# Kernel tuning notes

Hardware: AMD Instinct MI355X
Metric: run time of the kernel (lower is better)

Reference implementation:

```python
import jax, jax.numpy as jnp
import numpy as np

NUM_EMBEDDINGS = 8192
EMA_DECAY = 0.99


def setup_inputs() -> dict:
    key = jax.random.key(0)
    k1, k2 = jax.random.split(key)
    encodings = jax.random.normal(k1, (16, 128, 32, 32), dtype=jnp.float32)
    weight = 0.02 * jax.random.normal(k2, (NUM_EMBEDDINGS, 128), dtype=jnp.float32)
    return {"encodings": encodings, "weight": weight}


def reference(encodings, weight):
    B, C, H, W = encodings.shape
    K = weight.shape[0]
    # [B, C, H, W] -> [N, C], N = B*H*W
    x = encodings.transpose(0, 2, 3, 1).reshape(-1, C)
    # pairwise squared distances via norms + matmul: [N, K]
    dist = (
        jnp.sum(x * x, axis=1, keepdims=True)
        + jnp.sum(weight * weight, axis=1)[None, :]
        - 2.0 * jnp.matmul(x, weight.T)
    )
    quantized_ids = jnp.argmin(dist, axis=1)  # [N] int
    # straight-through estimator
    q = x + jax.lax.stop_gradient(weight[quantized_ids] - x)  # [N, C]
    # training-mode EMA codebook update (scatter-add counts and sums)
    counts = jax.ops.segment_sum(
        jnp.ones((x.shape[0],), dtype=x.dtype), quantized_ids, num_segments=K
    )
    sums = jax.ops.segment_sum(x, quantized_ids, num_segments=K)
    new_means = sums / (counts[:, None] + 1e-12)
    new_weight = EMA_DECAY * weight + (1.0 - EMA_DECAY) * new_means
    ids_out = quantized_ids.reshape(B, H, W)
    q_out = q.reshape(B, H, W, C).transpose(0, 3, 1, 2)  # [B, C, H, W]
    return ids_out, q_out, new_weight
```

## Files before the change

### kernel.cpp

```cpp
#include <hip/hip_runtime.h>
#include <stdint.h>
#include <stddef.h>


#define N_ROWS   16384
#define K_CODES  8192
#define C_DIM    128

typedef _Float16 f16x8 __attribute__((ext_vector_type(8)));
typedef float    f32x4 __attribute__((ext_vector_type(4)));

__global__ __launch_bounds__(256) void prep(const float* __restrict__ enc,
                                            const float* __restrict__ w,
                                            _Float16* __restrict__ Ap,
                                            _Float16* __restrict__ Bp,
                                            float* __restrict__ xT,
                                            float* __restrict__ xnorm,
                                            float* __restrict__ wnorm,
                                            float* __restrict__ wnmax128) {
  __shared__ float t[128][65];
  const int tid = threadIdx.x;
  if (blockIdx.x < 256) {
    const int b = blockIdx.x >> 4;
    const int hw0 = (blockIdx.x & 15) << 6;
    #pragma unroll
    for (int i = 0; i < 32; ++i) {
      int idx = i * 256 + tid;
      int c = idx >> 6, hwl = idx & 63;
      t[c][hwl] = enc[((size_t)(b * 128 + c) << 10) + hw0 + hwl];
    }
    __syncthreads();
    const int r = tid >> 2, sub = tid & 3;
    const int n = (b << 10) + hw0 + r;
    const int R = n >> 4, m = n & 15;
    float s = 0.f;
    #pragma unroll
    for (int q = 0; q < 4; ++q) {
      f16x8 hv;
      float vv[8];
      #pragma unroll
      for (int e = 0; e < 8; ++e) {
        float v = t[sub * 32 + q * 8 + e][r];
        vv[e] = v;
        s += v * v;
        hv[e] = (_Float16)v;
      }
      *(f16x8*)(Ap + ((size_t)(R * 4 + sub) * 64 + (m + 16 * q)) * 8) = hv;
      *(float4*)(xT + (size_t)n * 128 + sub * 32 + q * 8) =
          (float4){vv[0], vv[1], vv[2], vv[3]};
      *(float4*)(xT + (size_t)n * 128 + sub * 32 + q * 8 + 4) =
          (float4){vv[4], vv[5], vv[6], vv[7]};
    }
    s += __shfl_xor(s, 1);
    s += __shfl_xor(s, 2);
    if (sub == 0) xnorm[n] = s;
  } else {
    __shared__ float wred[4];
    const int kk = (blockIdx.x - 256) * 64 + (tid >> 2), sub = tid & 3;
    const int R = kk >> 4, m = kk & 15;
    const float* base = w + (size_t)kk * C_DIM + sub * 32;
    float s = 0.f;
    #pragma unroll
    for (int q = 0; q < 4; ++q) {
      f16x8 hv;
      float4 va = *(const float4*)(base + q * 8);
      float4 vb = *(const float4*)(base + q * 8 + 4);
      float vv[8] = {va.x, va.y, va.z, va.w, vb.x, vb.y, vb.z, vb.w};
      #pragma unroll
      for (int e = 0; e < 8; ++e) { s += vv[e] * vv[e]; hv[e] = (_Float16)vv[e]; }
      *(f16x8*)(Bp + ((size_t)(R * 4 + sub) * 64 + (m + 16 * q)) * 8) = hv;
    }
    s += __shfl_xor(s, 1);
    s += __shfl_xor(s, 2);
    if (sub == 0) wnorm[kk] = s;
    float wx = s;
    #pragma unroll
    for (int st = 1; st <= 32; st <<= 1) wx = fmaxf(wx, __shfl_xor(wx, st));
    if ((tid & 63) == 0) wred[tid >> 6] = wx;
    __syncthreads();
    if (tid == 0)
      wnmax128[blockIdx.x - 256] =
          fmaxf(fmaxf(wred[0], wred[1]), fmaxf(wred[2], wred[3]));
  }
}

__global__ __launch_bounds__(512) void gemm_argmin(
    const _Float16* __restrict__ Ap, const _Float16* __restrict__ Bp,
    const float* __restrict__ wnorm,
    float* __restrict__ pd1, float* __restrict__ pd2,
    unsigned* __restrict__ icount, unsigned* __restrict__ fcount)
{
  __shared__ _Float16 sbuf[2][8192];
  const int tid = threadIdx.x;
  const int lane = tid & 63, wave = tid >> 6;
  const int m = lane & 15, q = lane >> 4;
  const int cs = blockIdx.x;
  const int row0 = blockIdx.y * 128;
  const int Tr = blockIdx.y * 8 + wave;

  if (cs == 0 && blockIdx.y == 0 && tid == 0) {
    *icount = 0u; *fcount = 0u;
  }

#define STAGE(b, hgn) do {                                                   \
    const size_t bh_ = ((size_t)((cs * 64 + (hgn) * 4) * 4) << 9);           \
    _Pragma("unroll")                                                        \
    for (int r_ = 0; r_ < 2; ++r_) {                                         \
      __builtin_amdgcn_global_load_lds(                                      \
          (const __attribute__((address_space(1))) void*)                    \
              (Bp + bh_ + ((size_t)(r_ * 512 + tid) << 3)),                  \
          (__attribute__((address_space(3))) void*)                          \
              (&sbuf[b][(r_ * 512 + tid) << 3]),                             \
          16, 0, 0);                                                         \
    }                                                                        \
  } while (0)

  f16x8 bx[4];
  #pragma unroll
  for (int kc = 0; kc < 4; ++kc)
    bx[kc] = *(const f16x8*)(Ap + (((size_t)Tr * 4 + kc) << 9) + (lane << 3));
  const int row = row0 + wave * 16 + m;
  const unsigned q5 = (unsigned)(q << 5);

  STAGE(0, 0);

  float c1 = 0.f, c2 = 0.f;
  for (int hg = 0; hg < 16; ++hg) {
    __syncthreads();
    if (hg < 15) STAGE((hg + 1) & 1, hg + 1);
    const _Float16* fb = &sbuf[hg & 1][0];
    const int half = hg & 1;
    f32x4 acc[4];
    #pragma unroll
    for (int t = 0; t < 4; ++t) acc[t] = (f32x4){0.f, 0.f, 0.f, 0.f};
    #pragma unroll
    for (int kc = 0; kc < 4; ++kc) {
      #pragma unroll
      for (int t = 0; t < 4; ++t) {
        f16x8 a = *(const f16x8*)(fb + ((t * 4 + kc) << 9) + (lane << 3));
        acc[t] = __builtin_amdgcn_mfma_f32_16x16x32_f16(a, bx[kc], acc[t], 0, 0, 0);
      }
    }
    float m1t[4], m2t[4];
    #pragma unroll
    for (int t = 0; t < 4; ++t) {
      const int tj = half * 4 + t;
      const int cb = (cs * 64 + hg * 4 + t) * 16 + 4 * q;
      float4 wnq = *(const float4*)(wnorm + cb);
      unsigned b0 = __float_as_uint(fmaf(-2.0f, acc[t][0], wnq.x)) & 0xFFFFFF80u;
      unsigned b1 = __float_as_uint(fmaf(-2.0f, acc[t][1], wnq.y)) & 0xFFFFFF80u;
      unsigned b2 = __float_as_uint(fmaf(-2.0f, acc[t][2], wnq.z)) & 0xFFFFFF80u;
      unsigned b3 = __float_as_uint(fmaf(-2.0f, acc[t][3], wnq.w)) & 0xFFFFFF80u;
      float v0 = __uint_as_float(b0);
      float v1 = __uint_as_float(b1 | 1u);
      float v2 = __uint_as_float(b2 | 2u);
      float v3 = __uint_as_float(b3 | 3u);
      float l1 = fminf(v0, v1), h1 = fmaxf(v0, v1);
      float l2 = fminf(v2, v3), h2 = fmaxf(v2, v3);
      float mm1 = fminf(l1, l2);
      float mm2 = fminf(fminf(h1, h2), fmaxf(l1, l2));
      m1t[t] = __uint_as_float(__float_as_uint(mm1) | (unsigned)(tj << 2));
      m2t[t] = mm2;
    }
    m2t[0] = fminf(fminf(m2t[0], m2t[1]), fmaxf(m1t[0], m1t[1]));
    m1t[0] = fminf(m1t[0], m1t[1]);
    m2t[2] = fminf(fminf(m2t[2], m2t[3]), fmaxf(m1t[2], m1t[3]));
    m1t[2] = fminf(m1t[2], m1t[3]);
    m2t[0] = fminf(fminf(m2t[0], m2t[2]), fmaxf(m1t[0], m1t[2]));
    m1t[0] = fminf(m1t[0], m1t[2]);
    if (half == 0) {
      c1 = m1t[0]; c2 = m2t[0];
    } else {
      c2 = fminf(fminf(c2, m2t[0]), fmaxf(c1, m1t[0]));
      c1 = fminf(c1, m1t[0]);
      float d1 = __uint_as_float(__float_as_uint(c1) | q5);
      float d2 = c2;
      #pragma unroll
      for (int s = 16; s <= 32; s <<= 1) {
        float o1 = __shfl_xor(d1, s), o2 = __shfl_xor(d2, s);
        d2 = fminf(fminf(d2, o2), fmaxf(d1, o1));
        d1 = fminf(d1, o1);
      }
      if (q == 0) {
        const int g = cs * 8 + (hg >> 1);
        size_t pi = (size_t)g * N_ROWS + row;
        pd1[pi] = d1;
        pd2[pi] = d2;
      }
    }
  }
#undef STAGE
}

__global__ __launch_bounds__(256) void classify(
    const float* __restrict__ pd1, const float* __restrict__ pd2,
    const float* __restrict__ xnorm, const float* __restrict__ wnmax128,
    int* __restrict__ ids, unsigned* __restrict__ items,
    unsigned* __restrict__ icount, int* __restrict__ fulll,
    unsigned* __restrict__ fcount, unsigned long long* __restrict__ keys,
    unsigned* __restrict__ cnt)
{
  __shared__ float wred[4];
  const int tid = threadIdx.x;
  const int gidx = blockIdx.x * 256 + tid;
  const int row = gidx >> 2, p = gidx & 3;
  if (p == 0) keys[row] = ~0ull;
  if (gidx < K_CODES) cnt[gidx] = 0u;
  float wv = wnmax128[tid & 127];
  #pragma unroll
  for (int st = 1; st <= 32; st <<= 1) wv = fmaxf(wv, __shfl_xor(wv, st));
  if ((tid & 63) == 0) wred[tid >> 6] = wv;
  __syncthreads();
  const float wm = fmaxf(fmaxf(wred[0], wred[1]), fmaxf(wred[2], wred[3]));

  float v1[16];
  float lmin = __builtin_inff();
  #pragma unroll
  for (int j = 0; j < 16; ++j) {
    v1[j] = pd1[(size_t)(p * 16 + j) * N_ROWS + row];
    lmin = fminf(lmin, v1[j]);
  }
  lmin = fminf(lmin, __shfl_xor(lmin, 1));
  lmin = fminf(lmin, __shfl_xor(lmin, 2));
  float twoE = 2.0f * (0.0029297f * sqrtf(xnorm[row] * wm) + 5e-4f);
  float T = lmin + twoE;
  bool full = false;
  int nc = 0;
  unsigned cands[6];
  #pragma unroll
  for (int j = 0; j < 16; ++j) {
    size_t i = (size_t)(p * 16 + j) * N_ROWS + row;
    if (pd2[i] <= T) { full = true; }
    else if (v1[j] <= T) {
      if (nc < 6) {
        unsigned ui = __float_as_uint(v1[j]) & 127u;
        unsigned g = (unsigned)(p * 16 + j);
        cands[nc++] = (g << 7) | (((ui >> 2) & 7u) << 4) |
                      ((ui >> 5) << 2) | (ui & 3u);
      } else full = true;
    }
  }
  unsigned fm = full ? 1u : 0u;
  int nct = nc;
  fm |= (unsigned)__shfl_xor((int)fm, 1); nct += __shfl_xor(nct, 1);
  fm |= (unsigned)__shfl_xor((int)fm, 2); nct += __shfl_xor(nct, 2);
  if (nct > 6) fm = 1u;
  if (fm) {
    if (p == 0) { unsigned fi = atomicAdd(fcount, 1u); fulll[fi] = row; }
  } else if (nct >= 2) {
    if (nc > 0) {
      unsigned base = atomicAdd(icount, (unsigned)nc);
      for (int i2 = 0; i2 < nc; ++i2)
        items[base + i2] = ((unsigned)row << 13) | cands[i2];
    }
  } else if (nc == 1) {
    ids[row] = (int)cands[0];
  }
}

__global__ __launch_bounds__(256) void refine(
    const float* __restrict__ xT, const float* __restrict__ w,
    const float* __restrict__ xnorm, const float* __restrict__ wnorm,
    const unsigned* __restrict__ items, const unsigned* __restrict__ icount,
    const int* __restrict__ fulll, const unsigned* __restrict__ fcount,
    unsigned long long* __restrict__ keys) {
  const int tid = threadIdx.x;
  const int lane = tid & 63, wave = tid >> 6;
  const unsigned ic = *icount;
  for (unsigned i = blockIdx.x * 256 + tid; i < ic; i += gridDim.x * 256) {
    unsigned it = items[i];
    int row = (int)(it >> 13), c = (int)(it & 8191u);
    const float* xb = xT + (size_t)row * C_DIM;
    const float* wk = w + (size_t)c * C_DIM;
    float s = 0.f;
    #pragma unroll 8
    for (int c4 = 0; c4 < 32; ++c4) {
      float4 xv = *(const float4*)(xb + c4 * 4);
      float4 wv = *(const float4*)(wk + c4 * 4);
      s = fmaf(xv.x, wv.x, s);
      s = fmaf(xv.y, wv.y, s);
      s = fmaf(xv.z, wv.z, s);
      s = fmaf(xv.w, wv.w, s);
    }
    float d = (xnorm[row] + wnorm[c]) - 2.0f * s;
    unsigned sb = __float_as_uint(d);
    sb = (sb >> 31) ? ~sb : (sb | 0x80000000u);
    unsigned long long key = ((unsigned long long)sb << 32) | (unsigned)c;
    atomicMin(&keys[row], key);
  }
  __shared__ __align__(16) float xs[128];
  __shared__ unsigned long long red[4];
  const unsigned nitems = *fcount * 8;
  for (unsigned item = blockIdx.x; item < nitems; item += gridDim.x) {
    const int row = fulll[item >> 3];
    const int slice = (int)(item & 7u);
    if (tid < 128)
      xs[tid] = xT[(size_t)row * C_DIM + tid];
    __syncthreads();
    const float xn = xnorm[row];
    const int k0 = slice * 1024 + tid * 4;
    float S[4];
    #pragma unroll
    for (int j = 0; j < 4; ++j) S[j] = 0.f;
    for (int c4 = 0; c4 < 32; ++c4) {
      float4 xv = *(const float4*)(&xs[c4 * 4]);
      #pragma unroll
      for (int j = 0; j < 4; ++j) {
        float4 wv = *(const float4*)(w + (size_t)(k0 + j) * C_DIM + c4 * 4);
        S[j] = fmaf(xv.x, wv.x, S[j]);
        S[j] = fmaf(xv.y, wv.y, S[j]);
        S[j] = fmaf(xv.z, wv.z, S[j]);
        S[j] = fmaf(xv.w, wv.w, S[j]);
      }
    }
    unsigned long long best = ~0ull;
    #pragma unroll
    for (int j = 0; j < 4; ++j) {
      float d = (xn + wnorm[k0 + j]) - 2.0f * S[j];
      unsigned sb = __float_as_uint(d);
      sb = (sb >> 31) ? ~sb : (sb | 0x80000000u);
      unsigned long long key = ((unsigned long long)sb << 32) | (unsigned)(k0 + j);
      best = best < key ? best : key;
    }
    #pragma unroll
    for (int s = 1; s <= 32; s <<= 1) {
      unsigned long long ok = __shfl_xor(best, s);
      best = ok < best ? ok : best;
    }
    if (lane == 0) red[wave] = best;
    __syncthreads();
    if (tid == 0) {
      unsigned long long bk = red[0];
      #pragma unroll
      for (int wv = 1; wv < 4; ++wv) bk = red[wv] < bk ? red[wv] : bk;
      atomicMin(&keys[row], bk);
    }
    __syncthreads();
  }
}

__global__ void resolve_ids(const unsigned long long* __restrict__ keys,
                            int* __restrict__ ids, unsigned* __restrict__ cnt,
                            float* __restrict__ out_ids) {
  int row = blockIdx.x * 256 + threadIdx.x;
  unsigned long long k = keys[row];
  int id = (k != ~0ull) ? (int)(unsigned)(k & 0xffffffffu) : ids[row];
  ids[row] = id;
  out_ids[row] = (float)id;
  atomicAdd(&cnt[id], 1u);
}

__global__ __launch_bounds__(256) void scan_offsets(
    const unsigned* __restrict__ cnt,
    unsigned* __restrict__ offs, unsigned* __restrict__ cursor) {
  __shared__ unsigned tot[256];
  const int tid = threadIdx.x;
  unsigned local[32], run = 0;
  #pragma unroll
  for (int i = 0; i < 32; ++i) { local[i] = run; run += cnt[tid * 32 + i]; }
  tot[tid] = run;
  __syncthreads();
  for (int st = 1; st < 256; st <<= 1) {
    unsigned v = (tid >= st) ? tot[tid - st] : 0u;
    __syncthreads();
    tot[tid] += v;
    __syncthreads();
  }
  unsigned excl = (tid == 0) ? 0u : tot[tid - 1];
  #pragma unroll
  for (int i = 0; i < 32; ++i) {
    unsigned o = excl + local[i];
    offs[tid * 32 + i] = o;
    cursor[tid * 32 + i] = o;
  }
}

__global__ void fill_rowlist(const int* __restrict__ ids,
                             unsigned* __restrict__ cursor,
                             int* __restrict__ rowlist) {
  int row = blockIdx.x * 256 + threadIdx.x;
  unsigned slot = atomicAdd(&cursor[ids[row]], 1u);
  rowlist[slot] = row;
}

__global__ __launch_bounds__(256) void qsum_final(
    const float* __restrict__ enc, const float* __restrict__ w,
    const int* __restrict__ ids,
    const unsigned* __restrict__ cnt, const unsigned* __restrict__ offs,
    const int* __restrict__ rowlist, const float* __restrict__ xT,
    float* __restrict__ outq, float* __restrict__ outw) {
  if (blockIdx.x < 2048) {
    int e = blockIdx.x * 1024 + threadIdx.x * 4;
    int c = (e >> 10) & 127;
    int b = e >> 17;
    int n = (b << 10) | (e & 1023);
    float4 x = *(const float4*)(enc + e);
    float4 o;
    o.x = x.x + (w[(size_t)ids[n + 0] * C_DIM + c] - x.x);
    o.y = x.y + (w[(size_t)ids[n + 1] * C_DIM + c] - x.y);
    o.z = x.z + (w[(size_t)ids[n + 2] * C_DIM + c] - x.z);
    o.w = x.w + (w[(size_t)ids[n + 3] * C_DIM + c] - x.w);
    *(float4*)(outq + e) = o;
  } else {
    const int tid = threadIdx.x;
    const int lane = tid & 63, wave = tid >> 6;
    const int k = (int)(blockIdx.x - 2048) * 4 + wave;
    const unsigned n0 = offs[k], nk = cnt[k];
    float S0a = 0.f, S0b = 0.f, S0c = 0.f, S0d = 0.f;
    float S1a = 0.f, S1b = 0.f, S1c = 0.f, S1d = 0.f;
    unsigned i = 0;
    for (; i + 4 <= nk; i += 4) {
      int r0 = rowlist[n0 + i],     r1 = rowlist[n0 + i + 1];
      int r2 = rowlist[n0 + i + 2], r3 = rowlist[n0 + i + 3];
      S0a += xT[(size_t)r0 * 128 + lane];      S1a += xT[(size_t)r0 * 128 + lane + 64];
      S0b += xT[(size_t)r1 * 128 + lane];      S1b += xT[(size_t)r1 * 128 + lane + 64];
      S0c += xT[(size_t)r2 * 128 + lane];      S1c += xT[(size_t)r2 * 128 + lane + 64];
      S0d += xT[(size_t)r3 * 128 + lane];      S1d += xT[(size_t)r3 * 128 + lane + 64];
    }
    for (; i < nk; ++i) {
      int r = rowlist[n0 + i];
      S0a += xT[(size_t)r * 128 + lane];
      S1a += xT[(size_t)r * 128 + lane + 64];
    }
    float S0 = (S0a + S0b) + (S0c + S0d);
    float S1 = (S1a + S1b) + (S1c + S1d);
    const float omd = (float)(1.0 - 0.99);
    float cf = (float)nk + 1e-12f;
    outw[(size_t)k * 128 + lane]      = 0.99f * w[(size_t)k * 128 + lane]      + omd * (S0 / cf);
    outw[(size_t)k * 128 + lane + 64] = 0.99f * w[(size_t)k * 128 + lane + 64] + omd * (S1 / cf);
  }
}

extern "C" void kernel_launch(void* const* d_in, const int* in_sizes, int n_in,
                              void* d_out, int out_size, void* d_ws, size_t ws_size,
                              hipStream_t stream) {
  const float* enc = (const float*)d_in[0];
  const float* w   = (const float*)d_in[1];
  float* out = (float*)d_out;
  float* out_ids = out;
  float* out_q   = out + N_ROWS;
  float* out_w   = out + N_ROWS + N_ROWS * C_DIM;

  char* ws = (char*)d_ws;
  _Float16* Ap  = (_Float16*)(ws);
  _Float16* Bp  = (_Float16*)(ws + 4194304);
  float* xnorm  = (float*)(ws + 6291456);
  float* wnorm  = (float*)(ws + 6356992);
  float* pd1    = (float*)(ws + 6389760);
  float* pd2    = (float*)(ws + 10584064);
  float* wnmax128 = (float*)(ws + 14778368);
  int* ids      = (int*)(ws + 18972672);
  int* fulll    = (int*)(ws + 19038208);
  unsigned* items = (unsigned*)(ws + 19103744);
  unsigned* icount = (unsigned*)(ws + 20152324);
  unsigned* fcount = (unsigned*)(ws + 20152328);
  unsigned* cnt    = (unsigned*)(ws + 20152336);
  unsigned* offs   = (unsigned*)(ws + 20185104);
  unsigned* cursor = (unsigned*)(ws + 20217872);
  unsigned long long* keys = (unsigned long long*)(ws + 20250640);
  int* rowlist  = (int*)(ws + 20381712);
  float* xT     = (float*)(ws + 20447248);
  (void)in_sizes; (void)n_in; (void)out_size; (void)ws_size;


  prep<<<384, 256, 0, stream>>>(enc, w, Ap, Bp, xT, xnorm, wnorm, wnmax128);
  gemm_argmin<<<dim3(8, N_ROWS / 128), 512, 0, stream>>>(
      Ap, Bp, wnorm, pd1, pd2, icount, fcount);
  classify<<<N_ROWS * 4 / 256, 256, 0, stream>>>(
      pd1, pd2, xnorm, wnmax128, ids, items, icount, fulll, fcount, keys, cnt);
  refine<<<2048, 256, 0, stream>>>(xT, w, xnorm, wnorm, items, icount, fulll,
                                   fcount, keys);
  resolve_ids<<<N_ROWS / 256, 256, 0, stream>>>(keys, ids, cnt, out_ids);
  scan_offsets<<<1, 256, 0, stream>>>(cnt, offs, cursor);
  fill_rowlist<<<N_ROWS / 256, 256, 0, stream>>>(ids, cursor, rowlist);
  qsum_final<<<2048 + K_CODES / 4, 256, 0, stream>>>(
      enc, w, ids, cnt, offs, rowlist, xT, out_q, out_w);
}
```

Measured before the change: 207.8 us.

## Give each GEMM wave two row tiles and interleave partial-min output per row

Each wave in gemm_argmin now handles two 16-row A tiles that share every LDS-loaded B fragment. This doubles MFMA work per shared-memory read and halves the grid. The per-group min/second-min pairs move from two column-major arrays into one row-major interleaved buffer written as float2. Classify now uses one thread per row, reads it with contiguous float4 loads and needs no cross-lane shuffles. The cost is higher register pressure in the GEMM, fewer blocks for occupancy, and strided writes from the GEMM.

```diff
diff --git a/kernel.cpp b/kernel.cpp
--- a/kernel.cpp
+++ b/kernel.cpp
@@ -87,7 +87,7 @@
 __global__ __launch_bounds__(512) void gemm_argmin(
     const _Float16* __restrict__ Ap, const _Float16* __restrict__ Bp,
     const float* __restrict__ wnorm,
-    float* __restrict__ pd1, float* __restrict__ pd2,
+    float* __restrict__ pdx,
     unsigned* __restrict__ icount, unsigned* __restrict__ fcount)
 {
   __shared__ _Float16 sbuf[2][8192];
@@ -95,8 +95,7 @@
   const int lane = tid & 63, wave = tid >> 6;
   const int m = lane & 15, q = lane >> 4;
   const int cs = blockIdx.x;
-  const int row0 = blockIdx.y * 128;
-  const int Tr = blockIdx.y * 8 + wave;
+  const int TrA = blockIdx.y * 16 + wave * 2;
 
   if (cs == 0 && blockIdx.y == 0 && tid == 0) {
     *icount = 0u; *fcount = 0u;
@@ -115,77 +114,115 @@
     }                                                                        \
   } while (0)
 
-  f16x8 bx[4];
+  f16x8 bxA[4], bxB[4];
   #pragma unroll
-  for (int kc = 0; kc < 4; ++kc)
-    bx[kc] = *(const f16x8*)(Ap + (((size_t)Tr * 4 + kc) << 9) + (lane << 3));
-  const int row = row0 + wave * 16 + m;
+  for (int kc = 0; kc < 4; ++kc) {
+    bxA[kc] = *(const f16x8*)(Ap + (((size_t)TrA * 4 + kc) << 9) + (lane << 3));
+    bxB[kc] = *(const f16x8*)(Ap + (((size_t)(TrA + 1) * 4 + kc) << 9) + (lane << 3));
+  }
+  const int rowA = blockIdx.y * 256 + wave * 32 + m;
+  const int rowB = rowA + 16;
   const unsigned q5 = (unsigned)(q << 5);
 
   STAGE(0, 0);
 
-  float c1 = 0.f, c2 = 0.f;
+  float c1A = 0.f, c2A = 0.f, c1B = 0.f, c2B = 0.f;
   for (int hg = 0; hg < 16; ++hg) {
     __syncthreads();
     if (hg < 15) STAGE((hg + 1) & 1, hg + 1);
     const _Float16* fb = &sbuf[hg & 1][0];
     const int half = hg & 1;
-    f32x4 acc[4];
-    #pragma unroll
-    for (int t = 0; t < 4; ++t) acc[t] = (f32x4){0.f, 0.f, 0.f, 0.f};
+    f32x4 aA[4], aB[4];
+    #pragma unroll
+    for (int t = 0; t < 4; ++t) {
+      aA[t] = (f32x4){0.f, 0.f, 0.f, 0.f};
+      aB[t] = (f32x4){0.f, 0.f, 0.f, 0.f};
+    }
     #pragma unroll
     for (int kc = 0; kc < 4; ++kc) {
       #pragma unroll
       for (int t = 0; t < 4; ++t) {
         f16x8 a = *(const f16x8*)(fb + ((t * 4 + kc) << 9) + (lane << 3));
-        acc[t] = __builtin_amdgcn_mfma_f32_16x16x32_f16(a, bx[kc], acc[t], 0, 0, 0);
-      }
-    }
-    float m1t[4], m2t[4];
+        aA[t] = __builtin_amdgcn_mfma_f32_16x16x32_f16(a, bxA[kc], aA[t], 0, 0, 0);
+        aB[t] = __builtin_amdgcn_mfma_f32_16x16x32_f16(a, bxB[kc], aB[t], 0, 0, 0);
+      }
+    }
+    float m1A[4], m2A[4], m1B[4], m2B[4];
     #pragma unroll
     for (int t = 0; t < 4; ++t) {
       const int tj = half * 4 + t;
       const int cb = (cs * 64 + hg * 4 + t) * 16 + 4 * q;
       float4 wnq = *(const float4*)(wnorm + cb);
-      unsigned b0 = __float_as_uint(fmaf(-2.0f, acc[t][0], wnq.x)) & 0xFFFFFF80u;
-      unsigned b1 = __float_as_uint(fmaf(-2.0f, acc[t][1], wnq.y)) & 0xFFFFFF80u;
-      unsigned b2 = __float_as_uint(fmaf(-2.0f, acc[t][2], wnq.z)) & 0xFFFFFF80u;
-      unsigned b3 = __float_as_uint(fmaf(-2.0f, acc[t][3], wnq.w)) & 0xFFFFFF80u;
-      float v0 = __uint_as_float(b0);
-      float v1 = __uint_as_float(b1 | 1u);
-      float v2 = __uint_as_float(b2 | 2u);
-      float v3 = __uint_as_float(b3 | 3u);
-      float l1 = fminf(v0, v1), h1 = fmaxf(v0, v1);
-      float l2 = fminf(v2, v3), h2 = fmaxf(v2, v3);
-      float mm1 = fminf(l1, l2);
-      float mm2 = fminf(fminf(h1, h2), fmaxf(l1, l2));
-      m1t[t] = __uint_as_float(__float_as_uint(mm1) | (unsigned)(tj << 2));
-      m2t[t] = mm2;
-    }
-    m2t[0] = fminf(fminf(m2t[0], m2t[1]), fmaxf(m1t[0], m1t[1]));
-    m1t[0] = fminf(m1t[0], m1t[1]);
-    m2t[2] = fminf(fminf(m2t[2], m2t[3]), fmaxf(m1t[2], m1t[3]));
-    m1t[2] = fminf(m1t[2], m1t[3]);
-    m2t[0] = fminf(fminf(m2t[0], m2t[2]), fmaxf(m1t[0], m1t[2]));
-    m1t[0] = fminf(m1t[0], m1t[2]);
+      {
+        unsigned b0 = __float_as_uint(fmaf(-2.0f, aA[t][0], wnq.x)) & 0xFFFFFF80u;
+        unsigned b1 = __float_as_uint(fmaf(-2.0f, aA[t][1], wnq.y)) & 0xFFFFFF80u;
+        unsigned b2 = __float_as_uint(fmaf(-2.0f, aA[t][2], wnq.z)) & 0xFFFFFF80u;
+        unsigned b3 = __float_as_uint(fmaf(-2.0f, aA[t][3], wnq.w)) & 0xFFFFFF80u;
+        float v0 = __uint_as_float(b0);
+        float v1 = __uint_as_float(b1 | 1u);
+        float v2 = __uint_as_float(b2 | 2u);
+        float v3 = __uint_as_float(b3 | 3u);
+        float l1 = fminf(v0, v1), h1 = fmaxf(v0, v1);
+        float l2 = fminf(v2, v3), h2 = fmaxf(v2, v3);
+        float mm1 = fminf(l1, l2);
+        float mm2 = fminf(fminf(h1, h2), fmaxf(l1, l2));
+        m1A[t] = __uint_as_float(__float_as_uint(mm1) | (unsigned)(tj << 2));
+        m2A[t] = mm2;
+      }
+      {
+        unsigned b0 = __float_as_uint(fmaf(-2.0f, aB[t][0], wnq.x)) & 0xFFFFFF80u;
+        unsigned b1 = __float_as_uint(fmaf(-2.0f, aB[t][1], wnq.y)) & 0xFFFFFF80u;
+        unsigned b2 = __float_as_uint(fmaf(-2.0f, aB[t][2], wnq.z)) & 0xFFFFFF80u;
+        unsigned b3 = __float_as_uint(fmaf(-2.0f, aB[t][3], wnq.w)) & 0xFFFFFF80u;
+        float v0 = __uint_as_float(b0);
+        float v1 = __uint_as_float(b1 | 1u);
+        float v2 = __uint_as_float(b2 | 2u);
+        float v3 = __uint_as_float(b3 | 3u);
+        float l1 = fminf(v0, v1), h1 = fmaxf(v0, v1);
+        float l2 = fminf(v2, v3), h2 = fmaxf(v2, v3);
+        float mm1 = fminf(l1, l2);
+        float mm2 = fminf(fminf(h1, h2), fmaxf(l1, l2));
+        m1B[t] = __uint_as_float(__float_as_uint(mm1) | (unsigned)(tj << 2));
+        m2B[t] = mm2;
+      }
+    }
+    m2A[0] = fminf(fminf(m2A[0], m2A[1]), fmaxf(m1A[0], m1A[1]));
+    m1A[0] = fminf(m1A[0], m1A[1]);
+    m2A[2] = fminf(fminf(m2A[2], m2A[3]), fmaxf(m1A[2], m1A[3]));
+    m1A[2] = fminf(m1A[2], m1A[3]);
+    m2A[0] = fminf(fminf(m2A[0], m2A[2]), fmaxf(m1A[0], m1A[2]));
+    m1A[0] = fminf(m1A[0], m1A[2]);
+    m2B[0] = fminf(fminf(m2B[0], m2B[1]), fmaxf(m1B[0], m1B[1]));
+    m1B[0] = fminf(m1B[0], m1B[1]);
+    m2B[2] = fminf(fminf(m2B[2], m2B[3]), fmaxf(m1B[2], m1B[3]));
+    m1B[2] = fminf(m1B[2], m1B[3]);
+    m2B[0] = fminf(fminf(m2B[0], m2B[2]), fmaxf(m1B[0], m1B[2]));
+    m1B[0] = fminf(m1B[0], m1B[2]);
     if (half == 0) {
-      c1 = m1t[0]; c2 = m2t[0];
+      c1A = m1A[0]; c2A = m2A[0];
+      c1B = m1B[0]; c2B = m2B[0];
     } else {
-      c2 = fminf(fminf(c2, m2t[0]), fmaxf(c1, m1t[0]));
-      c1 = fminf(c1, m1t[0]);
-      float d1 = __uint_as_float(__float_as_uint(c1) | q5);
-      float d2 = c2;
+      c2A = fminf(fminf(c2A, m2A[0]), fmaxf(c1A, m1A[0]));
+      c1A = fminf(c1A, m1A[0]);
+      c2B = fminf(fminf(c2B, m2B[0]), fmaxf(c1B, m1B[0]));
+      c1B = fminf(c1B, m1B[0]);
+      float d1A = __uint_as_float(__float_as_uint(c1A) | q5);
+      float d2A = c2A;
+      float d1B = __uint_as_float(__float_as_uint(c1B) | q5);
+      float d2B = c2B;
       #pragma unroll
       for (int s = 16; s <= 32; s <<= 1) {
-        float o1 = __shfl_xor(d1, s), o2 = __shfl_xor(d2, s);
-        d2 = fminf(fminf(d2, o2), fmaxf(d1, o1));
-        d1 = fminf(d1, o1);
+        float o1 = __shfl_xor(d1A, s), o2 = __shfl_xor(d2A, s);
+        d2A = fminf(fminf(d2A, o2), fmaxf(d1A, o1));
+        d1A = fminf(d1A, o1);
+        float p1 = __shfl_xor(d1B, s), p2 = __shfl_xor(d2B, s);
+        d2B = fminf(fminf(d2B, p2), fmaxf(d1B, p1));
+        d1B = fminf(d1B, p1);
       }
       if (q == 0) {
         const int g = cs * 8 + (hg >> 1);
-        size_t pi = (size_t)g * N_ROWS + row;
-        pd1[pi] = d1;
-        pd2[pi] = d2;
+        *(float2*)(pdx + ((size_t)rowA << 7) + 2 * g) = (float2){d1A, d2A};
+        *(float2*)(pdx + ((size_t)rowB << 7) + 2 * g) = (float2){d1B, d2B};
       }
     }
   }
@@ -193,7 +230,7 @@
 }
 
 __global__ __launch_bounds__(256) void classify(
-    const float* __restrict__ pd1, const float* __restrict__ pd2,
+    const float* __restrict__ pdx,
     const float* __restrict__ xnorm, const float* __restrict__ wnmax128,
     int* __restrict__ ids, unsigned* __restrict__ items,
     unsigned* __restrict__ icount, int* __restrict__ fulll,
@@ -202,10 +239,9 @@
 {
   __shared__ float wred[4];
   const int tid = threadIdx.x;
-  const int gidx = blockIdx.x * 256 + tid;
-  const int row = gidx >> 2, p = gidx & 3;
-  if (p == 0) keys[row] = ~0ull;
-  if (gidx < K_CODES) cnt[gidx] = 0u;
+  const int row = blockIdx.x * 256 + tid;
+  keys[row] = ~0ull;
+  if (row < K_CODES) cnt[row] = 0u;
   float wv = wnmax128[tid & 127];
   #pragma unroll
   for (int st = 1; st <= 32; st <<= 1) wv = fmaxf(wv, __shfl_xor(wv, st));
@@ -213,47 +249,48 @@
   __syncthreads();
   const float wm = fmaxf(fmaxf(wred[0], wred[1]), fmaxf(wred[2], wred[3]));
 
-  float v1[16];
+  const float* pr = pdx + ((size_t)row << 7);
   float lmin = __builtin_inff();
   #pragma unroll
-  for (int j = 0; j < 16; ++j) {
-    v1[j] = pd1[(size_t)(p * 16 + j) * N_ROWS + row];
-    lmin = fminf(lmin, v1[j]);
-  }
-  lmin = fminf(lmin, __shfl_xor(lmin, 1));
-  lmin = fminf(lmin, __shfl_xor(lmin, 2));
+  for (int j = 0; j < 32; ++j) {
+    float4 v = *(const float4*)(pr + j * 4);
+    lmin = fminf(lmin, fminf(v.x, v.z));
+  }
   float twoE = 2.0f * (0.0029297f * sqrtf(xnorm[row] * wm) + 5e-4f);
   float T = lmin + twoE;
   bool full = false;
   int nc = 0;
   unsigned cands[6];
   #pragma unroll
-  for (int j = 0; j < 16; ++j) {
-    size_t i = (size_t)(p * 16 + j) * N_ROWS + row;
-    if (pd2[i] <= T) { full = true; }
-    else if (v1[j] <= T) {
+  for (int j = 0; j < 32; ++j) {
+    float4 v = *(const float4*)(pr + j * 4);
+    if (v.y <= T) { full = true; }
+    else if (v.x <= T) {
       if (nc < 6) {
-        unsigned ui = __float_as_uint(v1[j]) & 127u;
-        unsigned g = (unsigned)(p * 16 + j);
+        unsigned ui = __float_as_uint(v.x) & 127u;
+        unsigned g = (unsigned)(2 * j);
         cands[nc++] = (g << 7) | (((ui >> 2) & 7u) << 4) |
                       ((ui >> 5) << 2) | (ui & 3u);
       } else full = true;
     }
-  }
-  unsigned fm = full ? 1u : 0u;
-  int nct = nc;
-  fm |= (unsigned)__shfl_xor((int)fm, 1); nct += __shfl_xor(nct, 1);
-  fm |= (unsigned)__shfl_xor((int)fm, 2); nct += __shfl_xor(nct, 2);
-  if (nct > 6) fm = 1u;
-  if (fm) {
-    if (p == 0) { unsigned fi = atomicAdd(fcount, 1u); fulll[fi] = row; }
-  } else if (nct >= 2) {
-    if (nc > 0) {
-      unsigned base = atomicAdd(icount, (unsigned)nc);
-      for (int i2 = 0; i2 < nc; ++i2)
-        items[base + i2] = ((unsigned)row << 13) | cands[i2];
-    }
-  } else if (nc == 1) {
+    if (v.w <= T) { full = true; }
+    else if (v.z <= T) {
+      if (nc < 6) {
+        unsigned ui = __float_as_uint(v.z) & 127u;
+        unsigned g = (unsigned)(2 * j + 1);
+        cands[nc++] = (g << 7) | (((ui >> 2) & 7u) << 4) |
+                      ((ui >> 5) << 2) | (ui & 3u);
+      } else full = true;
+    }
+  }
+  if (full) {
+    unsigned fi = atomicAdd(fcount, 1u);
+    fulll[fi] = row;
+  } else if (nc >= 2) {
+    unsigned base = atomicAdd(icount, (unsigned)nc);
+    for (int i2 = 0; i2 < nc; ++i2)
+      items[base + i2] = ((unsigned)row << 13) | cands[i2];
+  } else {
     ids[row] = (int)cands[0];
   }
 }
@@ -446,8 +483,7 @@
   _Float16* Bp  = (_Float16*)(ws + 4194304);
   float* xnorm  = (float*)(ws + 6291456);
   float* wnorm  = (float*)(ws + 6356992);
-  float* pd1    = (float*)(ws + 6389760);
-  float* pd2    = (float*)(ws + 10584064);
+  float* pdx    = (float*)(ws + 6389760);
   float* wnmax128 = (float*)(ws + 14778368);
   int* ids      = (int*)(ws + 18972672);
   int* fulll    = (int*)(ws + 19038208);
@@ -464,10 +500,10 @@
 
 
   prep<<<384, 256, 0, stream>>>(enc, w, Ap, Bp, xT, xnorm, wnorm, wnmax128);
-  gemm_argmin<<<dim3(8, N_ROWS / 128), 512, 0, stream>>>(
-      Ap, Bp, wnorm, pd1, pd2, icount, fcount);
-  classify<<<N_ROWS * 4 / 256, 256, 0, stream>>>(
-      pd1, pd2, xnorm, wnmax128, ids, items, icount, fulll, fcount, keys, cnt);
+  gemm_argmin<<<dim3(8, N_ROWS / 256), 512, 0, stream>>>(
+      Ap, Bp, wnorm, pdx, icount, fcount);
+  classify<<<N_ROWS / 256, 256, 0, stream>>>(
+      pdx, xnorm, wnmax128, ids, items, icount, fulll, fcount, keys, cnt);
   refine<<<2048, 256, 0, stream>>>(xT, w, xnorm, wnorm, items, icount, fulll,
                                    fcount, keys);
   resolve_ids<<<N_ROWS / 256, 256, 0, stream>>>(keys, ids, cnt, out_ids);
```

Result: no change. 211.0 us (+1.5%).

## Refine ambiguous rows per 64-code group instead of full 8192-code rescans

Applied to the files above, without the earlier changes.

The GEMM epilogue now emits per-64-code-group top-2 partials (finer granularity), storing the second-min as a rounded-up bf16-like 16-bit value to halve its traffic. Classify flags only the specific groups whose second-min or overflow candidates fall under the threshold, pushing (row, group) entries into a hit list instead of marking the whole row for full rescan. Refine then checks just 64 codes per hit entry, replacing the 8192-code full-row fallback, with an items cap that spills to the hit list. This trades more partial-writes and atomics in classify for far less exact-fallback work.

```diff
diff --git a/kernel.cpp b/kernel.cpp
--- a/kernel.cpp
+++ b/kernel.cpp
@@ -6,6 +6,7 @@
 #define N_ROWS   16384
 #define K_CODES  8192
 #define C_DIM    128
+#define ITEMS_CAP 32768u
 
 typedef _Float16 f16x8 __attribute__((ext_vector_type(8)));
 typedef float    f32x4 __attribute__((ext_vector_type(4)));
@@ -87,8 +88,8 @@
 __global__ __launch_bounds__(512) void gemm_argmin(
     const _Float16* __restrict__ Ap, const _Float16* __restrict__ Bp,
     const float* __restrict__ wnorm,
-    float* __restrict__ pd1, float* __restrict__ pd2,
-    unsigned* __restrict__ icount, unsigned* __restrict__ fcount)
+    float* __restrict__ pd1h, unsigned short* __restrict__ pd2h,
+    unsigned* __restrict__ icount, unsigned* __restrict__ hcount)
 {
   __shared__ _Float16 sbuf[2][8192];
   const int tid = threadIdx.x;
@@ -99,7 +100,7 @@
   const int Tr = blockIdx.y * 8 + wave;
 
   if (cs == 0 && blockIdx.y == 0 && tid == 0) {
-    *icount = 0u; *fcount = 0u;
+    *icount = 0u; *hcount = 0u;
   }
 
 #define STAGE(b, hgn) do {                                                   \
@@ -120,16 +121,14 @@
   for (int kc = 0; kc < 4; ++kc)
     bx[kc] = *(const f16x8*)(Ap + (((size_t)Tr * 4 + kc) << 9) + (lane << 3));
   const int row = row0 + wave * 16 + m;
-  const unsigned q5 = (unsigned)(q << 5);
+  const unsigned q2 = (unsigned)(q << 2);
 
   STAGE(0, 0);
 
-  float c1 = 0.f, c2 = 0.f;
   for (int hg = 0; hg < 16; ++hg) {
     __syncthreads();
     if (hg < 15) STAGE((hg + 1) & 1, hg + 1);
     const _Float16* fb = &sbuf[hg & 1][0];
-    const int half = hg & 1;
     f32x4 acc[4];
     #pragma unroll
     for (int t = 0; t < 4; ++t) acc[t] = (f32x4){0.f, 0.f, 0.f, 0.f};
@@ -144,23 +143,21 @@
     float m1t[4], m2t[4];
     #pragma unroll
     for (int t = 0; t < 4; ++t) {
-      const int tj = half * 4 + t;
       const int cb = (cs * 64 + hg * 4 + t) * 16 + 4 * q;
       float4 wnq = *(const float4*)(wnorm + cb);
-      unsigned b0 = __float_as_uint(fmaf(-2.0f, acc[t][0], wnq.x)) & 0xFFFFFF80u;
-      unsigned b1 = __float_as_uint(fmaf(-2.0f, acc[t][1], wnq.y)) & 0xFFFFFF80u;
-      unsigned b2 = __float_as_uint(fmaf(-2.0f, acc[t][2], wnq.z)) & 0xFFFFFF80u;
-      unsigned b3 = __float_as_uint(fmaf(-2.0f, acc[t][3], wnq.w)) & 0xFFFFFF80u;
+      const unsigned e0 = (unsigned)(t << 4);
+      unsigned b0 = (__float_as_uint(fmaf(-2.0f, acc[t][0], wnq.x)) & 0xFFFFFFC0u) | e0;
+      unsigned b1 = (__float_as_uint(fmaf(-2.0f, acc[t][1], wnq.y)) & 0xFFFFFFC0u) | (e0 | 1u);
+      unsigned b2 = (__float_as_uint(fmaf(-2.0f, acc[t][2], wnq.z)) & 0xFFFFFFC0u) | (e0 | 2u);
+      unsigned b3 = (__float_as_uint(fmaf(-2.0f, acc[t][3], wnq.w)) & 0xFFFFFFC0u) | (e0 | 3u);
       float v0 = __uint_as_float(b0);
-      float v1 = __uint_as_float(b1 | 1u);
-      float v2 = __uint_as_float(b2 | 2u);
-      float v3 = __uint_as_float(b3 | 3u);
+      float v1 = __uint_as_float(b1);
+      float v2 = __uint_as_float(b2);
+      float v3 = __uint_as_float(b3);
       float l1 = fminf(v0, v1), h1 = fmaxf(v0, v1);
       float l2 = fminf(v2, v3), h2 = fmaxf(v2, v3);
-      float mm1 = fminf(l1, l2);
-      float mm2 = fminf(fminf(h1, h2), fmaxf(l1, l2));
-      m1t[t] = __uint_as_float(__float_as_uint(mm1) | (unsigned)(tj << 2));
-      m2t[t] = mm2;
+      m1t[t] = fminf(l1, l2);
+      m2t[t] = fminf(fminf(h1, h2), fmaxf(l1, l2));
     }
     m2t[0] = fminf(fminf(m2t[0], m2t[1]), fmaxf(m1t[0], m1t[1]));
     m1t[0] = fminf(m1t[0], m1t[1]);
@@ -168,36 +165,31 @@
     m1t[2] = fminf(m1t[2], m1t[3]);
     m2t[0] = fminf(fminf(m2t[0], m2t[2]), fmaxf(m1t[0], m1t[2]));
     m1t[0] = fminf(m1t[0], m1t[2]);
-    if (half == 0) {
-      c1 = m1t[0]; c2 = m2t[0];
-    } else {
-      c2 = fminf(fminf(c2, m2t[0]), fmaxf(c1, m1t[0]));
-      c1 = fminf(c1, m1t[0]);
-      float d1 = __uint_as_float(__float_as_uint(c1) | q5);
-      float d2 = c2;
-      #pragma unroll
-      for (int s = 16; s <= 32; s <<= 1) {
-        float o1 = __shfl_xor(d1, s), o2 = __shfl_xor(d2, s);
-        d2 = fminf(fminf(d2, o2), fmaxf(d1, o1));
-        d1 = fminf(d1, o1);
-      }
-      if (q == 0) {
-        const int g = cs * 8 + (hg >> 1);
-        size_t pi = (size_t)g * N_ROWS + row;
-        pd1[pi] = d1;
-        pd2[pi] = d2;
-      }
+    float d1 = __uint_as_float(__float_as_uint(m1t[0]) | q2);
+    float d2 = __uint_as_float(__float_as_uint(m2t[0]) | q2);
+    #pragma unroll
+    for (int s = 16; s <= 32; s <<= 1) {
+      float o1 = __shfl_xor(d1, s), o2 = __shfl_xor(d2, s);
+      d2 = fminf(fminf(d2, o2), fmaxf(d1, o1));
+      d1 = fminf(d1, o1);
+    }
+    if (q == 0) {
+      const int h = cs * 16 + hg;
+      pd1h[(size_t)h * N_ROWS + row] = d1;
+      unsigned bb = __float_as_uint(d2);
+      bb += ((unsigned)((int)bb >> 31)) & 0xFFFFu;
+      pd2h[(size_t)h * N_ROWS + row] = (unsigned short)(bb >> 16);
     }
   }
 #undef STAGE
 }
 
 __global__ __launch_bounds__(256) void classify(
-    const float* __restrict__ pd1, const float* __restrict__ pd2,
+    const float* __restrict__ pd1h, const unsigned short* __restrict__ pd2h,
     const float* __restrict__ xnorm, const float* __restrict__ wnmax128,
     int* __restrict__ ids, unsigned* __restrict__ items,
-    unsigned* __restrict__ icount, int* __restrict__ fulll,
-    unsigned* __restrict__ fcount, unsigned long long* __restrict__ keys,
+    unsigned* __restrict__ icount, unsigned* __restrict__ hlist,
+    unsigned* __restrict__ hcount, unsigned long long* __restrict__ keys,
     unsigned* __restrict__ cnt)
 {
   __shared__ float wred[4];
@@ -213,48 +205,53 @@
   __syncthreads();
   const float wm = fmaxf(fmaxf(wred[0], wred[1]), fmaxf(wred[2], wred[3]));
 
-  float v1[16];
+  float v1[32];
   float lmin = __builtin_inff();
   #pragma unroll
-  for (int j = 0; j < 16; ++j) {
-    v1[j] = pd1[(size_t)(p * 16 + j) * N_ROWS + row];
+  for (int j = 0; j < 32; ++j) {
+    v1[j] = pd1h[(size_t)(p * 32 + j) * N_ROWS + row];
     lmin = fminf(lmin, v1[j]);
   }
   lmin = fminf(lmin, __shfl_xor(lmin, 1));
   lmin = fminf(lmin, __shfl_xor(lmin, 2));
   float twoE = 2.0f * (0.0029297f * sqrtf(xnorm[row] * wm) + 5e-4f);
   float T = lmin + twoE;
-  bool full = false;
-  int nc = 0;
+  int nc = 0, hr = 0;
   unsigned cands[6];
-  #pragma unroll
-  for (int j = 0; j < 16; ++j) {
-    size_t i = (size_t)(p * 16 + j) * N_ROWS + row;
-    if (pd2[i] <= T) { full = true; }
-    else if (v1[j] <= T) {
+  #pragma unroll 8
+  for (int j = 0; j < 32; ++j) {
+    const int h = p * 32 + j;
+    float p2 = __uint_as_float(
+        (unsigned)pd2h[(size_t)h * N_ROWS + row] << 16);
+    if (p2 <= T) {
+      unsigned hi = atomicAdd(hcount, 1u);
+      hlist[hi] = ((unsigned)row << 7) | (unsigned)h;
+      hr++;
+    } else if (v1[j] <= T) {
       if (nc < 6) {
-        unsigned ui = __float_as_uint(v1[j]) & 127u;
-        unsigned g = (unsigned)(p * 16 + j);
-        cands[nc++] = (g << 7) | (((ui >> 2) & 7u) << 4) |
-                      ((ui >> 5) << 2) | (ui & 3u);
-      } else full = true;
-    }
-  }
-  unsigned fm = full ? 1u : 0u;
-  int nct = nc;
-  fm |= (unsigned)__shfl_xor((int)fm, 1); nct += __shfl_xor(nct, 1);
-  fm |= (unsigned)__shfl_xor((int)fm, 2); nct += __shfl_xor(nct, 2);
-  if (nct > 6) fm = 1u;
-  if (fm) {
-    if (p == 0) { unsigned fi = atomicAdd(fcount, 1u); fulll[fi] = row; }
-  } else if (nct >= 2) {
-    if (nc > 0) {
-      unsigned base = atomicAdd(icount, (unsigned)nc);
+        cands[nc++] = (unsigned)h * 64u + (__float_as_uint(v1[j]) & 63u);
+      } else {
+        unsigned hi = atomicAdd(hcount, 1u);
+        hlist[hi] = ((unsigned)row << 7) | (unsigned)h;
+        hr++;
+      }
+    }
+  }
+  int nct = nc + __shfl_xor(nc, 1); nct += __shfl_xor(nct, 2);
+  int hrt = hr + __shfl_xor(hr, 1); hrt += __shfl_xor(hrt, 2);
+  if (hrt == 0 && nct == 1) {
+    if (nc == 1) ids[row] = (int)cands[0];
+  } else if (nc > 0) {
+    unsigned base = atomicAdd(icount, (unsigned)nc);
+    if (base + (unsigned)nc <= ITEMS_CAP) {
       for (int i2 = 0; i2 < nc; ++i2)
         items[base + i2] = ((unsigned)row << 13) | cands[i2];
-    }
-  } else if (nc == 1) {
-    ids[row] = (int)cands[0];
+    } else {
+      for (int i2 = 0; i2 < nc; ++i2) {
+        unsigned hi = atomicAdd(hcount, 1u);
+        hlist[hi] = ((unsigned)row << 7) | (cands[i2] >> 6);
+      }
+    }
   }
 }
 
@@ -262,12 +259,13 @@
     const float* __restrict__ xT, const float* __restrict__ w,
     const float* __restrict__ xnorm, const float* __restrict__ wnorm,
     const unsigned* __restrict__ items, const unsigned* __restrict__ icount,
-    const int* __restrict__ fulll, const unsigned* __restrict__ fcount,
+    const unsigned* __restrict__ hlist, const unsigned* __restrict__ hcount,
     unsigned long long* __restrict__ keys) {
   const int tid = threadIdx.x;
   const int lane = tid & 63, wave = tid >> 6;
   const unsigned ic = *icount;
-  for (unsigned i = blockIdx.x * 256 + tid; i < ic; i += gridDim.x * 256) {
+  const unsigned ica = ic <= ITEMS_CAP ? ic : ITEMS_CAP;
+  for (unsigned i = blockIdx.x * 256 + tid; i < ica; i += gridDim.x * 256) {
     unsigned it = items[i];
     int row = (int)(it >> 13), c = (int)(it & 8191u);
     const float* xb = xT + (size_t)row * C_DIM;
@@ -290,41 +288,38 @@
   }
   __shared__ __align__(16) float xs[128];
   __shared__ unsigned long long red[4];
-  const unsigned nitems = *fcount * 8;
-  for (unsigned item = blockIdx.x; item < nitems; item += gridDim.x) {
-    const int row = fulll[item >> 3];
-    const int slice = (int)(item & 7u);
+  const unsigned hc = *hcount;
+  for (unsigned item = blockIdx.x; item < hc; item += gridDim.x) {
+    const unsigned e = hlist[item];
+    const int row = (int)(e >> 7), h = (int)(e & 127u);
     if (tid < 128)
       xs[tid] = xT[(size_t)row * C_DIM + tid];
     __syncthreads();
-    const float xn = xnorm[row];
-    const int k0 = slice * 1024 + tid * 4;
-    float S[4];
-    #pragma unroll
-    for (int j = 0; j < 4; ++j) S[j] = 0.f;
-    for (int c4 = 0; c4 < 32; ++c4) {
-      float4 xv = *(const float4*)(&xs[c4 * 4]);
-      #pragma unroll
-      for (int j = 0; j < 4; ++j) {
-        float4 wv = *(const float4*)(w + (size_t)(k0 + j) * C_DIM + c4 * 4);
-        S[j] = fmaf(xv.x, wv.x, S[j]);
-        S[j] = fmaf(xv.y, wv.y, S[j]);
-        S[j] = fmaf(xv.z, wv.z, S[j]);
-        S[j] = fmaf(xv.w, wv.w, S[j]);
-      }
-    }
+    const int code = h * 64 + (tid >> 2);
+    const int qt = tid & 3;
+    const float* wk = w + (size_t)code * C_DIM + qt * 32;
+    float s = 0.f;
+    #pragma unroll
+    for (int c4 = 0; c4 < 8; ++c4) {
+      float4 wv = *(const float4*)(wk + c4 * 4);
+      float4 xv = *(const float4*)(&xs[qt * 32 + c4 * 4]);
+      s = fmaf(xv.x, wv.x, s);
+      s = fmaf(xv.y, wv.y, s);
+      s = fmaf(xv.z, wv.z, s);
+      s = fmaf(xv.w, wv.w, s);
+    }
+    s += __shfl_xor(s, 1);
+    s += __shfl_xor(s, 2);
     unsigned long long best = ~0ull;
-    #pragma unroll
-    for (int j = 0; j < 4; ++j) {
-      float d = (xn + wnorm[k0 + j]) - 2.0f * S[j];
+    if (qt == 0) {
+      float d = (xnorm[row] + wnorm[code]) - 2.0f * s;
       unsigned sb = __float_as_uint(d);
       sb = (sb >> 31) ? ~sb : (sb | 0x80000000u);
-      unsigned long long key = ((unsigned long long)sb << 32) | (unsigned)(k0 + j);
-      best = best < key ? best : key;
-    }
-    #pragma unroll
-    for (int s = 1; s <= 32; s <<= 1) {
-      unsigned long long ok = __shfl_xor(best, s);
+      best = ((unsigned long long)sb << 32) | (unsigned)code;
+    }
+    #pragma unroll
+    for (int st = 1; st <= 32; st <<= 1) {
+      unsigned long long ok = __shfl_xor(best, st);
       best = ok < best ? ok : best;
     }
     if (lane == 0) red[wave] = best;
@@ -446,30 +441,31 @@
   _Float16* Bp  = (_Float16*)(ws + 4194304);
   float* xnorm  = (float*)(ws + 6291456);
   float* wnorm  = (float*)(ws + 6356992);
-  float* pd1    = (float*)(ws + 6389760);
-  float* pd2    = (float*)(ws + 10584064);
-  float* wnmax128 = (float*)(ws + 14778368);
-  int* ids      = (int*)(ws + 18972672);
-  int* fulll    = (int*)(ws + 19038208);
-  unsigned* items = (unsigned*)(ws + 19103744);
-  unsigned* icount = (unsigned*)(ws + 20152324);
-  unsigned* fcount = (unsigned*)(ws + 20152328);
-  unsigned* cnt    = (unsigned*)(ws + 20152336);
-  unsigned* offs   = (unsigned*)(ws + 20185104);
-  unsigned* cursor = (unsigned*)(ws + 20217872);
-  unsigned long long* keys = (unsigned long long*)(ws + 20250640);
-  int* rowlist  = (int*)(ws + 20381712);
+  float* pd1h   = (float*)(ws + 6389760);
+  unsigned short* pd2h = (unsigned short*)(ws + 14778368);
+  float* wnmax128 = (float*)(ws + 18972672);
+  int* ids      = (int*)(ws + 18973184);
+  unsigned* hlist = (unsigned*)(ws + 19038720);
+  unsigned* items = (unsigned*)(ws + 19563008);
+  unsigned* icount = (unsigned*)(ws + 19694080);
+  unsigned* hcount = (unsigned*)(ws + 19694084);
+  unsigned* cnt    = (unsigned*)(ws + 19694096);
+  unsigned* offs   = (unsigned*)(ws + 19726864);
+  unsigned* cursor = (unsigned*)(ws + 19759632);
+  unsigned long long* keys = (unsigned long long*)(ws + 19792400);
+  int* rowlist  = (int*)(ws + 19923472);
   float* xT     = (float*)(ws + 20447248);
   (void)in_sizes; (void)n_in; (void)out_size; (void)ws_size;
 
 
   prep<<<384, 256, 0, stream>>>(enc, w, Ap, Bp, xT, xnorm, wnorm, wnmax128);
   gemm_argmin<<<dim3(8, N_ROWS / 128), 512, 0, stream>>>(
-      Ap, Bp, wnorm, pd1, pd2, icount, fcount);
+      Ap, Bp, wnorm, pd1h, pd2h, icount, hcount);
   classify<<<N_ROWS * 4 / 256, 256, 0, stream>>>(
-      pd1, pd2, xnorm, wnmax128, ids, items, icount, fulll, fcount, keys, cnt);
-  refine<<<2048, 256, 0, stream>>>(xT, w, xnorm, wnorm, items, icount, fulll,
-                                   fcount, keys);
+      pd1h, pd2h, xnorm, wnmax128, ids, items, icount, hlist, hcount,
+      keys, cnt);
+  refine<<<2048, 256, 0, stream>>>(xT, w, xnorm, wnorm, items, icount,
+                                   hlist, hcount, keys);
   resolve_ids<<<N_ROWS / 256, 256, 0, stream>>>(keys, ids, cnt, out_ids);
   scan_offsets<<<1, 256, 0, stream>>>(cnt, offs, cursor);
   fill_rowlist<<<N_ROWS / 256, 256, 0, stream>>>(ids, cursor, rowlist);
```

Measured after the change: 187.5 us (median of 2 runs). -9.7%, faster.
